# Performance work log

Measured on AMD Instinct MI355X. Metric: run time of the kernel, lower is better.

Reference implementation:

```python
import jax, jax.numpy as jnp
import numpy as np

HEADS = 16
KV_HEADS = 4
HEAD_DIM = 64
EMBED = 1024


def setup_inputs() -> dict:
    key = jax.random.key(0)
    k1, k2, k3, k4, k5 = jax.random.split(key, 5)
    B, S, G, E = 1, 2048, 2, EMBED
    scale = 1.0 / np.sqrt(E)
    x = jax.random.normal(k1, (B, S, G, E), dtype=jnp.float32)
    Wq = jax.random.normal(k2, (E, HEADS * HEAD_DIM), dtype=jnp.float32) * scale
    Wk = jax.random.normal(k3, (E, KV_HEADS * HEAD_DIM), dtype=jnp.float32) * scale
    Wv = jax.random.normal(k4, (E, KV_HEADS * HEAD_DIM), dtype=jnp.float32) * scale
    Wo = jax.random.normal(k5, (E, E), dtype=jnp.float32) * scale
    return {"x": x, "Wq": Wq, "Wk": Wk, "Wv": Wv, "Wo": Wo}


def reference(x, Wq, Wk, Wv, Wo):
    B, S, G, E = x.shape
    ratio = HEADS // KV_HEADS
    # projections over last dim (no bias, no activation)
    q = (x @ Wq).reshape(B, S, G, HEADS, HEAD_DIM)
    k = (x @ Wk).reshape(B, S, G, KV_HEADS, HEAD_DIM)
    v = (x @ Wv).reshape(B, S, G, KV_HEADS, HEAD_DIM)
    # GQA repeat_kv: each kv head repeated `ratio` times consecutively
    k = jnp.repeat(k, ratio, axis=3)  # [B,S,G,H,D]
    v = jnp.repeat(v, ratio, axis=3)
    # energy: [B,G,H,Q,K]
    energy = jnp.einsum('bqghd,bkghd->bghqk', q, k)
    # causal mask: triu(1) set to -inf (before the sqrt scaling, as in source)
    causal = jnp.triu(jnp.ones((S, S), dtype=bool), 1)
    energy = jnp.where(causal, -jnp.inf, energy)
    scores = jax.nn.softmax(energy / np.sqrt(HEAD_DIM), axis=-1)
    attn = jnp.einsum('bghqv,bvghd->bqghd', scores, v)
    attn = attn.reshape(B, S, G, E)
    return attn @ Wo
```

## Files before the change

kernel.cpp:

```cpp
#include <hip/hip_runtime.h>
#include <cstdint>
#include <cstddef>

typedef __bf16 bf16_t;
typedef bf16_t bf16x8 __attribute__((ext_vector_type(8)));
typedef float f32x4 __attribute__((ext_vector_type(4)));

__device__ inline bf16x8 load8(const float* p) {
  f32x4 a = *reinterpret_cast<const f32x4*>(p);
  f32x4 b = *reinterpret_cast<const f32x4*>(p + 4);
  bf16x8 r;
  r[0] = (bf16_t)a[0]; r[1] = (bf16_t)a[1];
  r[2] = (bf16_t)a[2]; r[3] = (bf16_t)a[3];
  r[4] = (bf16_t)b[0]; r[5] = (bf16_t)b[1];
  r[6] = (bf16_t)b[2]; r[7] = (bf16_t)b[3];
  return r;
}
__device__ inline bf16x8 load8(const bf16_t* p) {
  return *reinterpret_cast<const bf16x8*>(p);
}

__global__ __launch_bounds__(256) void cvtx_k(const float* __restrict__ x,
                                              bf16_t* __restrict__ xb) {
  const size_t i = (size_t)blockIdx.x * 2048 + (size_t)threadIdx.x * 8;
  *reinterpret_cast<bf16x8*>(xb + i) = load8(x + i);
}

__global__ __launch_bounds__(256) void cvtT_k(
    const float* __restrict__ Wq, const float* __restrict__ Wk,
    const float* __restrict__ Wv, const float* __restrict__ Wo,
    bf16_t* __restrict__ wqT, bf16_t* __restrict__ wkT,
    bf16_t* __restrict__ wvT, bf16_t* __restrict__ woT) {
  __shared__ bf16_t Ts[64][72];
  const int b = blockIdx.x;
  const float* S;
  bf16_t* D;
  int N, idx;
  if (b < 256) { S = Wq; D = wqT; N = 1024; idx = b; }
  else if (b < 320) { S = Wk; D = wkT; N = 256; idx = b - 256; }
  else if (b < 384) { S = Wv; D = wvT; N = 256; idx = b - 320; }
  else { S = Wo; D = woT; N = 1024; idx = b - 384; }
  const int ntl = (N == 1024) ? 4 : 2;
  const int kt0 = (idx >> ntl) * 64;
  const int n0 = (idx & ((1 << ntl) - 1)) * 64;
  const int tid = threadIdx.x;
#pragma unroll
  for (int i = 0; i < 2; ++i) {
    const int c = tid + 256 * i;
    const int row = c >> 3, col0 = (c & 7) * 8;
    *reinterpret_cast<bf16x8*>(&Ts[row][col0]) =
        load8(&S[(size_t)(kt0 + row) * N + n0 + col0]);
  }
  __syncthreads();
#pragma unroll
  for (int i = 0; i < 2; ++i) {
    const int c = tid + 256 * i;
    const int nrow = c >> 3, k0 = (c & 7) * 8;
    bf16x8 v;
#pragma unroll
    for (int j = 0; j < 8; ++j) v[j] = Ts[k0 + j][nrow];
    *reinterpret_cast<bf16x8*>(&D[(size_t)(n0 + nrow) * 1024 + kt0 + k0]) = v;
  }
}

template <typename OutT>
__device__ inline void gemm_bt_body(const bf16_t* __restrict__ A,
                                    const bf16_t* __restrict__ BT,
                                    OutT* __restrict__ C, int m0, int bt0,
                                    int K, int CN, int cn0, float alpha) {
  __shared__ __align__(16) bf16_t As[128][40];
  __shared__ __align__(16) bf16_t Bs[128][40];

  const int tid = threadIdx.x;
  const int wave = tid >> 6, lane = tid & 63;
  const int quad = lane >> 4, l16 = lane & 15;
  const int moff = (wave & 1) * 64, noff = (wave >> 1) * 64;

  f32x4 acc[4][4];
#pragma unroll
  for (int mt = 0; mt < 4; ++mt)
#pragma unroll
    for (int nt = 0; nt < 4; ++nt) acc[mt][nt] = {0.f, 0.f, 0.f, 0.f};

  const int arow = tid >> 1, ak0 = (tid & 1) * 16;

  bf16x8 a0, a1, b0, b1;
  {
    const bf16_t* ap = &A[(size_t)(m0 + arow) * K + ak0];
    a0 = load8(ap); a1 = load8(ap + 8);
    const bf16_t* bp = &BT[(size_t)(bt0 + arow) * K + ak0];
    b0 = load8(bp); b1 = load8(bp + 8);
  }

  for (int k0 = 0; k0 < K; k0 += 32) {
    *reinterpret_cast<bf16x8*>(&As[arow][ak0]) = a0;
    *reinterpret_cast<bf16x8*>(&As[arow][ak0 + 8]) = a1;
    *reinterpret_cast<bf16x8*>(&Bs[arow][ak0]) = b0;
    *reinterpret_cast<bf16x8*>(&Bs[arow][ak0 + 8]) = b1;
    __syncthreads();
    if (k0 + 32 < K) {
      const bf16_t* ap = &A[(size_t)(m0 + arow) * K + k0 + 32 + ak0];
      a0 = load8(ap); a1 = load8(ap + 8);
      const bf16_t* bp = &BT[(size_t)(bt0 + arow) * K + k0 + 32 + ak0];
      b0 = load8(bp); b1 = load8(bp + 8);
    }
    bf16x8 af[4], bfr[4];
#pragma unroll
    for (int mt = 0; mt < 4; ++mt)
      af[mt] =
          *reinterpret_cast<const bf16x8*>(&As[moff + mt * 16 + l16][quad * 8]);
#pragma unroll
    for (int nt = 0; nt < 4; ++nt)
      bfr[nt] =
          *reinterpret_cast<const bf16x8*>(&Bs[noff + nt * 16 + l16][quad * 8]);
#pragma unroll
    for (int mt = 0; mt < 4; ++mt)
#pragma unroll
      for (int nt = 0; nt < 4; ++nt)
        acc[mt][nt] = __builtin_amdgcn_mfma_f32_16x16x32_bf16(
            af[mt], bfr[nt], acc[mt][nt], 0, 0, 0);
    __syncthreads();
  }

#pragma unroll
  for (int mt = 0; mt < 4; ++mt) {
    const int crow = m0 + moff + mt * 16 + quad * 4;
#pragma unroll
    for (int nt = 0; nt < 4; ++nt) {
      const int ccol = cn0 + noff + nt * 16 + l16;
#pragma unroll
      for (int r = 0; r < 4; ++r)
        C[(size_t)(crow + r) * CN + ccol] = (OutT)(acc[mt][nt][r] * alpha);
    }
  }
}

__global__ __launch_bounds__(256, 3) void qkv_k(
    const bf16_t* __restrict__ x, const bf16_t* __restrict__ wqT,
    const bf16_t* __restrict__ wkT, const bf16_t* __restrict__ wvT,
    bf16_t* __restrict__ Qo, bf16_t* __restrict__ Ko, bf16_t* __restrict__ Vo) {
  const int n0 = blockIdx.x * 128;
  const int m0 = blockIdx.y * 128;
  const bf16_t* BT;
  bf16_t* C;
  int CN, bn0;
  float alpha;
  if (n0 < 1024) {
    BT = wqT; C = Qo; CN = 1024; bn0 = n0; alpha = 0.125f;
  } else if (n0 < 1280) {
    BT = wkT; C = Ko; CN = 256; bn0 = n0 - 1024; alpha = 1.0f;
  } else {
    BT = wvT; C = Vo; CN = 256; bn0 = n0 - 1280; alpha = 1.0f;
  }
  gemm_bt_body<bf16_t>(x, BT, C, m0, bn0, 1024, CN, bn0, alpha);
}

template <typename OutT>
__global__ __launch_bounds__(256, 3) void gemm_bt_k(
    const bf16_t* __restrict__ A, const bf16_t* __restrict__ BT,
    OutT* __restrict__ C, int K, int N, float alpha) {
  gemm_bt_body<OutT>(A, BT, C, blockIdx.y * 128, blockIdx.x * 128, K, N,
                     blockIdx.x * 128, alpha);
}

__global__ __launch_bounds__(256) void transpose_v_k(
    const bf16_t* __restrict__ V, bf16_t* __restrict__ VT) {
  __shared__ bf16_t Vs[64][72];
  const int tid = threadIdx.x;
  const int kt0 = blockIdx.x * 64;
  const int ghk = blockIdx.y;
  const int g = ghk >> 2, kh = ghk & 3;
#pragma unroll
  for (int i = 0; i < 2; ++i) {
    const int c = tid + 256 * i;
    const int row = c >> 3, d0 = (c & 7) * 8;
    *reinterpret_cast<bf16x8*>(&Vs[row][d0]) = *reinterpret_cast<const bf16x8*>(
        &V[((size_t)(kt0 + row) * 2 + g) * 256 + kh * 64 + d0]);
  }
  __syncthreads();
#pragma unroll
  for (int i = 0; i < 2; ++i) {
    const int c = tid + 256 * i;
    const int d = c >> 3, k0 = (c & 7) * 8;
    bf16x8 v;
#pragma unroll
    for (int j = 0; j < 8; ++j) v[j] = Vs[k0 + j][d];
    *reinterpret_cast<bf16x8*>(&VT[((size_t)ghk * 64 + d) * 2048 + kt0 + k0]) =
        v;
  }
}

__global__ __launch_bounds__(128, 2) void flash6_k(
    const bf16_t* __restrict__ Q, const bf16_t* __restrict__ K,
    const bf16_t* __restrict__ VT, bf16_t* __restrict__ ATTN) {
  __shared__ __align__(16) bf16_t Ks[64][64];
  __shared__ __align__(16) bf16_t Vs[64][64];
  __shared__ __align__(16) bf16_t Ps[2][32][64];

  const int tid = threadIdx.x;
  const int w = tid >> 6, lane = tid & 63;
  const int quad = lane >> 4, l16 = lane & 15;
  const int b = blockIdx.x;
  const int j8 = b & 7, i8 = b >> 3;
  const int T = (i8 == 0) ? j8
              : (i8 == 1) ? (15 - j8)
              : (i8 == 2) ? (16 + j8)
                          : (31 - j8);
  const int gh = blockIdx.y;
  const int g = gh >> 4, h = gh & 15, kh = h >> 2;
  const int qbase = T * 64 + w * 32;
  const int swz = ((l16 >> 2) & 3) << 4;
  const int rsw = l16 & 7;

  bf16x8 qf[2][2];
#pragma unroll
  for (int rg = 0; rg < 2; ++rg)
#pragma unroll
    for (int t = 0; t < 2; ++t)
      qf[rg][t] = *reinterpret_cast<const bf16x8*>(
          &Q[((size_t)(qbase + rg * 16 + l16) * 2 + g) * 1024 + h * 64 +
             t * 32 + quad * 8]);

  f32x4 O[2][4];
  f32x4 lp[2];
#pragma unroll
  for (int rg = 0; rg < 2; ++rg) {
    lp[rg] = {0.f, 0.f, 0.f, 0.f};
#pragma unroll
    for (int d = 0; d < 4; ++d) O[rg][d] = {0.f, 0.f, 0.f, 0.f};
  }

  bf16x8 kr[4], vr[4];
#pragma unroll
  for (int i = 0; i < 4; ++i) {
    const int c = tid + 128 * i;
    const int row = c >> 3, e0 = (c & 7) * 8;
    kr[i] = *reinterpret_cast<const bf16x8*>(
        &K[((size_t)(row)*2 + g) * 256 + kh * 64 + e0]);
    vr[i] = *reinterpret_cast<const bf16x8*>(
        &VT[((size_t)(g * 4 + kh) * 64 + row) * 2048 + e0]);
  }

  for (int kt = 0; kt <= T; ++kt) {
#pragma unroll
    for (int i = 0; i < 4; ++i) {
      const int c = tid + 128 * i;
      const int row = c >> 3;
      const int pb = (((c & 7) ^ (row & 7)) << 3);
      *reinterpret_cast<bf16x8*>(&Ks[row][pb]) = kr[i];
      *reinterpret_cast<bf16x8*>(&Vs[row][pb]) = vr[i];
    }
    __syncthreads();
    if (kt < T) {
      const int nt0 = (kt + 1) * 64;
#pragma unroll
      for (int i = 0; i < 4; ++i) {
        const int c = tid + 128 * i;
        const int row = c >> 3, e0 = (c & 7) * 8;
        kr[i] = *reinterpret_cast<const bf16x8*>(
            &K[((size_t)(nt0 + row) * 2 + g) * 256 + kh * 64 + e0]);
        vr[i] = *reinterpret_cast<const bf16x8*>(
            &VT[((size_t)(g * 4 + kh) * 64 + row) * 2048 + nt0 + e0]);
      }
    }

    f32x4 s[2][4];
#pragma unroll
    for (int nt = 0; nt < 4; ++nt) {
      bf16x8 kf0 = *reinterpret_cast<const bf16x8*>(
          &Ks[nt * 16 + l16][(quad ^ rsw) << 3]);
      bf16x8 kf1 = *reinterpret_cast<const bf16x8*>(
          &Ks[nt * 16 + l16][((4 + quad) ^ rsw) << 3]);
#pragma unroll
      for (int rg = 0; rg < 2; ++rg) {
        f32x4 z = {0.f, 0.f, 0.f, 0.f};
        z = __builtin_amdgcn_mfma_f32_16x16x32_bf16(qf[rg][0], kf0, z, 0, 0, 0);
        s[rg][nt] =
            __builtin_amdgcn_mfma_f32_16x16x32_bf16(qf[rg][1], kf1, z, 0, 0, 0);
      }
    }
    const bool diag = (kt == T);
#pragma unroll
    for (int rg = 0; rg < 2; ++rg) {
#pragma unroll
      for (int nt = 0; nt < 4; ++nt) {
        const int key = nt * 16 + l16;
#pragma unroll
        for (int r = 0; r < 4; ++r) {
          float p = __expf(s[rg][nt][r]);
          if (diag && key > w * 32 + rg * 16 + quad * 4 + r) p = 0.f;
          lp[rg][r] += p;
          Ps[w][rg * 16 + quad * 4 + r][((nt ^ quad) << 4) + l16] = (bf16_t)p;
        }
      }
    }
    bf16x8 pf[2][2];
#pragma unroll
    for (int rg = 0; rg < 2; ++rg)
#pragma unroll
      for (int t = 0; t < 2; ++t)
        pf[rg][t] = *reinterpret_cast<const bf16x8*>(
            &Ps[w][rg * 16 + l16][(t * 32 + quad * 8) ^ swz]);
#pragma unroll
    for (int dnt = 0; dnt < 4; ++dnt) {
      bf16x8 vf0 = *reinterpret_cast<const bf16x8*>(
          &Vs[dnt * 16 + l16][(quad ^ rsw) << 3]);
      bf16x8 vf1 = *reinterpret_cast<const bf16x8*>(
          &Vs[dnt * 16 + l16][((4 + quad) ^ rsw) << 3]);
#pragma unroll
      for (int rg = 0; rg < 2; ++rg) {
        O[rg][dnt] = __builtin_amdgcn_mfma_f32_16x16x32_bf16(
            pf[rg][0], vf0, O[rg][dnt], 0, 0, 0);
        O[rg][dnt] = __builtin_amdgcn_mfma_f32_16x16x32_bf16(
            pf[rg][1], vf1, O[rg][dnt], 0, 0, 0);
      }
    }
    __syncthreads();
  }

#pragma unroll
  for (int rg = 0; rg < 2; ++rg) {
#pragma unroll
    for (int off = 1; off < 16; off <<= 1)
#pragma unroll
      for (int r = 0; r < 4; ++r) lp[rg][r] += __shfl_xor(lp[rg][r], off, 64);
#pragma unroll
    for (int r = 0; r < 4; ++r) {
      const float inv = 1.f / lp[rg][r];
      const int row = qbase + rg * 16 + quad * 4 + r;
#pragma unroll
      for (int dnt = 0; dnt < 4; ++dnt)
        ATTN[((size_t)row * 2 + g) * 1024 + h * 64 + dnt * 16 + l16] =
            (bf16_t)(O[rg][dnt][r] * inv);
    }
  }
}

extern "C" void kernel_launch(void* const* d_in, const int* in_sizes, int n_in,
                              void* d_out, int out_size, void* d_ws,
                              size_t ws_size, hipStream_t stream) {
  (void)in_sizes;
  (void)n_in;
  (void)out_size;
  (void)ws_size;

  const float* x = (const float*)d_in[0];
  const float* Wq = (const float*)d_in[1];
  const float* Wk = (const float*)d_in[2];
  const float* Wv = (const float*)d_in[3];
  const float* Wo = (const float*)d_in[4];
  float* out = (float*)d_out;

  const size_t MB = 1024 * 1024;
  char* ob = (char*)d_out;
  bf16_t* Qtmp = (bf16_t*)ob;
  bf16_t* VTws = (bf16_t*)(ob + 8 * MB);
  bf16_t* wqT = (bf16_t*)(ob + 10 * MB);
  bf16_t* wkT = (bf16_t*)(ob + 12 * MB);
  bf16_t* wvT = (bf16_t*)(ob + 12 * MB + 512 * 1024);
  bf16_t* Vws = (bf16_t*)(ob + 13 * MB);
  char* wb = (char*)d_ws;
  bf16_t* Kws = (bf16_t*)wb;
  bf16_t* woT = (bf16_t*)(wb + 2 * MB);
  bf16_t* ATTNws = (bf16_t*)(wb + 4 * MB);
  bf16_t* xb = ATTNws;

  cvtx_k<<<dim3(2048), dim3(256), 0, stream>>>(x, xb);
  cvtT_k<<<dim3(640), dim3(256), 0, stream>>>(Wq, Wk, Wv, Wo, wqT, wkT, wvT,
                                              woT);
  qkv_k<<<dim3(12, 32), dim3(256), 0, stream>>>(xb, wqT, wkT, wvT, Qtmp, Kws,
                                                Vws);
  transpose_v_k<<<dim3(32, 8), dim3(256), 0, stream>>>(Vws, VTws);
  flash6_k<<<dim3(32, 32), dim3(128), 0, stream>>>(Qtmp, Kws, VTws, ATTNws);
  gemm_bt_k<float><<<dim3(8, 32), dim3(256), 0, stream>>>(ATTNws, woT, out,
                                                          1024, 1024, 1.0f);
}
```

Baseline: 188.1 us.

## Halve flash attention query tile to double block count and add MFMA priority hints

The attention kernel now processes 32 query rows per block instead of 64, so each wave handles 16 rows, and the grid doubles to 64x32 blocks. The causal tile ordering is extended to 64 tiles and the diagonal mask is adjusted for the half-tile offset. This aims to improve occupancy and load balance on the causal triangle, at the cost of each K/V tile being loaded twice as often. It also adds s_setprio around the MFMA sections.

```diff
diff --git a/kernel.cpp b/kernel.cpp
--- a/kernel.cpp
+++ b/kernel.cpp
@@ -190,12 +190,12 @@
   }
 }
 
-__global__ __launch_bounds__(128, 2) void flash6_k(
+__global__ __launch_bounds__(128, 4) void flash7_k(
     const bf16_t* __restrict__ Q, const bf16_t* __restrict__ K,
     const bf16_t* __restrict__ VT, bf16_t* __restrict__ ATTN) {
   __shared__ __align__(16) bf16_t Ks[64][64];
   __shared__ __align__(16) bf16_t Vs[64][64];
-  __shared__ __align__(16) bf16_t Ps[2][32][64];
+  __shared__ __align__(16) bf16_t Ps[2][16][64];
 
   const int tid = threadIdx.x;
   const int w = tid >> 6, lane = tid & 63;
@@ -205,30 +205,29 @@
   const int T = (i8 == 0) ? j8
               : (i8 == 1) ? (15 - j8)
               : (i8 == 2) ? (16 + j8)
-                          : (31 - j8);
+              : (i8 == 3) ? (31 - j8)
+              : (i8 == 4) ? (32 + j8)
+              : (i8 == 5) ? (47 - j8)
+              : (i8 == 6) ? (48 + j8)
+                          : (63 - j8);
   const int gh = blockIdx.y;
   const int g = gh >> 4, h = gh & 15, kh = h >> 2;
-  const int qbase = T * 64 + w * 32;
+  const int qrow = T * 32 + w * 16;
+  const int Tk = T >> 1;
   const int swz = ((l16 >> 2) & 3) << 4;
   const int rsw = l16 & 7;
 
-  bf16x8 qf[2][2];
-#pragma unroll
-  for (int rg = 0; rg < 2; ++rg)
-#pragma unroll
-    for (int t = 0; t < 2; ++t)
-      qf[rg][t] = *reinterpret_cast<const bf16x8*>(
-          &Q[((size_t)(qbase + rg * 16 + l16) * 2 + g) * 1024 + h * 64 +
-             t * 32 + quad * 8]);
-
-  f32x4 O[2][4];
-  f32x4 lp[2];
-#pragma unroll
-  for (int rg = 0; rg < 2; ++rg) {
-    lp[rg] = {0.f, 0.f, 0.f, 0.f};
-#pragma unroll
-    for (int d = 0; d < 4; ++d) O[rg][d] = {0.f, 0.f, 0.f, 0.f};
-  }
+  bf16x8 qf[2];
+#pragma unroll
+  for (int t = 0; t < 2; ++t)
+    qf[t] = *reinterpret_cast<const bf16x8*>(
+        &Q[((size_t)(qrow + l16) * 2 + g) * 1024 + h * 64 + t * 32 +
+           quad * 8]);
+
+  f32x4 O[4];
+  f32x4 lp = {0.f, 0.f, 0.f, 0.f};
+#pragma unroll
+  for (int d = 0; d < 4; ++d) O[d] = {0.f, 0.f, 0.f, 0.f};
 
   bf16x8 kr[4], vr[4];
 #pragma unroll
@@ -241,7 +240,7 @@
         &VT[((size_t)(g * 4 + kh) * 64 + row) * 2048 + e0]);
   }
 
-  for (int kt = 0; kt <= T; ++kt) {
+  for (int kt = 0; kt <= Tk; ++kt) {
 #pragma unroll
     for (int i = 0; i < 4; ++i) {
       const int c = tid + 128 * i;
@@ -251,7 +250,7 @@
       *reinterpret_cast<bf16x8*>(&Vs[row][pb]) = vr[i];
     }
     __syncthreads();
-    if (kt < T) {
+    if (kt < Tk) {
       const int nt0 = (kt + 1) * 64;
 #pragma unroll
       for (int i = 0; i < 4; ++i) {
@@ -264,75 +263,65 @@
       }
     }
 
-    f32x4 s[2][4];
+    f32x4 s[4];
+    __builtin_amdgcn_s_setprio(1);
 #pragma unroll
     for (int nt = 0; nt < 4; ++nt) {
       bf16x8 kf0 = *reinterpret_cast<const bf16x8*>(
           &Ks[nt * 16 + l16][(quad ^ rsw) << 3]);
       bf16x8 kf1 = *reinterpret_cast<const bf16x8*>(
           &Ks[nt * 16 + l16][((4 + quad) ^ rsw) << 3]);
-#pragma unroll
-      for (int rg = 0; rg < 2; ++rg) {
-        f32x4 z = {0.f, 0.f, 0.f, 0.f};
-        z = __builtin_amdgcn_mfma_f32_16x16x32_bf16(qf[rg][0], kf0, z, 0, 0, 0);
-        s[rg][nt] =
-            __builtin_amdgcn_mfma_f32_16x16x32_bf16(qf[rg][1], kf1, z, 0, 0, 0);
+      f32x4 z = {0.f, 0.f, 0.f, 0.f};
+      z = __builtin_amdgcn_mfma_f32_16x16x32_bf16(qf[0], kf0, z, 0, 0, 0);
+      s[nt] = __builtin_amdgcn_mfma_f32_16x16x32_bf16(qf[1], kf1, z, 0, 0, 0);
+    }
+    __builtin_amdgcn_s_setprio(0);
+    const bool diag = (kt == Tk);
+    const int qloc = ((T & 1) << 5) + w * 16 + quad * 4;
+#pragma unroll
+    for (int nt = 0; nt < 4; ++nt) {
+      const int key = nt * 16 + l16;
+#pragma unroll
+      for (int r = 0; r < 4; ++r) {
+        float p = __expf(s[nt][r]);
+        if (diag && key > qloc + r) p = 0.f;
+        lp[r] += p;
+        Ps[w][quad * 4 + r][((nt ^ quad) << 4) + l16] = (bf16_t)p;
       }
     }
-    const bool diag = (kt == T);
-#pragma unroll
-    for (int rg = 0; rg < 2; ++rg) {
-#pragma unroll
-      for (int nt = 0; nt < 4; ++nt) {
-        const int key = nt * 16 + l16;
-#pragma unroll
-        for (int r = 0; r < 4; ++r) {
-          float p = __expf(s[rg][nt][r]);
-          if (diag && key > w * 32 + rg * 16 + quad * 4 + r) p = 0.f;
-          lp[rg][r] += p;
-          Ps[w][rg * 16 + quad * 4 + r][((nt ^ quad) << 4) + l16] = (bf16_t)p;
-        }
-      }
-    }
-    bf16x8 pf[2][2];
-#pragma unroll
-    for (int rg = 0; rg < 2; ++rg)
-#pragma unroll
-      for (int t = 0; t < 2; ++t)
-        pf[rg][t] = *reinterpret_cast<const bf16x8*>(
-            &Ps[w][rg * 16 + l16][(t * 32 + quad * 8) ^ swz]);
+    bf16x8 pf[2];
+#pragma unroll
+    for (int t = 0; t < 2; ++t)
+      pf[t] = *reinterpret_cast<const bf16x8*>(
+          &Ps[w][l16][(t * 32 + quad * 8) ^ swz]);
+    __builtin_amdgcn_s_setprio(1);
 #pragma unroll
     for (int dnt = 0; dnt < 4; ++dnt) {
       bf16x8 vf0 = *reinterpret_cast<const bf16x8*>(
           &Vs[dnt * 16 + l16][(quad ^ rsw) << 3]);
       bf16x8 vf1 = *reinterpret_cast<const bf16x8*>(
           &Vs[dnt * 16 + l16][((4 + quad) ^ rsw) << 3]);
-#pragma unroll
-      for (int rg = 0; rg < 2; ++rg) {
-        O[rg][dnt] = __builtin_amdgcn_mfma_f32_16x16x32_bf16(
-            pf[rg][0], vf0, O[rg][dnt], 0, 0, 0);
-        O[rg][dnt] = __builtin_amdgcn_mfma_f32_16x16x32_bf16(
-            pf[rg][1], vf1, O[rg][dnt], 0, 0, 0);
-      }
-    }
+      O[dnt] = __builtin_amdgcn_mfma_f32_16x16x32_bf16(pf[0], vf0, O[dnt], 0,
+                                                       0, 0);
+      O[dnt] = __builtin_amdgcn_mfma_f32_16x16x32_bf16(pf[1], vf1, O[dnt], 0,
+                                                       0, 0);
+    }
+    __builtin_amdgcn_s_setprio(0);
     __syncthreads();
   }
 
 #pragma unroll
-  for (int rg = 0; rg < 2; ++rg) {
-#pragma unroll
-    for (int off = 1; off < 16; off <<= 1)
-#pragma unroll
-      for (int r = 0; r < 4; ++r) lp[rg][r] += __shfl_xor(lp[rg][r], off, 64);
-#pragma unroll
-    for (int r = 0; r < 4; ++r) {
-      const float inv = 1.f / lp[rg][r];
-      const int row = qbase + rg * 16 + quad * 4 + r;
-#pragma unroll
-      for (int dnt = 0; dnt < 4; ++dnt)
-        ATTN[((size_t)row * 2 + g) * 1024 + h * 64 + dnt * 16 + l16] =
-            (bf16_t)(O[rg][dnt][r] * inv);
-    }
+  for (int off = 1; off < 16; off <<= 1)
+#pragma unroll
+    for (int r = 0; r < 4; ++r) lp[r] += __shfl_xor(lp[r], off, 64);
+#pragma unroll
+  for (int r = 0; r < 4; ++r) {
+    const float inv = 1.f / lp[r];
+    const int row = qrow + quad * 4 + r;
+#pragma unroll
+    for (int dnt = 0; dnt < 4; ++dnt)
+      ATTN[((size_t)row * 2 + g) * 1024 + h * 64 + dnt * 16 + l16] =
+          (bf16_t)(O[dnt][r] * inv);
   }
 }
 
@@ -371,7 +360,7 @@
   qkv_k<<<dim3(12, 32), dim3(256), 0, stream>>>(xb, wqT, wkT, wvT, Qtmp, Kws,
                                                 Vws);
   transpose_v_k<<<dim3(32, 8), dim3(256), 0, stream>>>(Vws, VTws);
-  flash6_k<<<dim3(32, 32), dim3(128), 0, stream>>>(Qtmp, Kws, VTws, ATTNws);
+  flash7_k<<<dim3(64, 32), dim3(128), 0, stream>>>(Qtmp, Kws, VTws, ATTNws);
   gemm_bt_k<float><<<dim3(8, 32), dim3(256), 0, stream>>>(ATTNws, woT, out,
                                                           1024, 1024, 1.0f);
 }
```

New measurement: 203.5 us. 1.08x slower.
